# Kernel tuning notes

Measured on AMD Instinct MI355X. Metric: run time of the kernel, lower is better.

## Reference

```python
import jax, jax.numpy as jnp
import numpy as np

N_NODES = 100000
N_EDGES = 1600000
HIDDEN = 64


def setup_inputs() -> dict:
    key = jax.random.key(0)
    k1, k2, k3, k4 = jax.random.split(key, 4)
    x = jax.random.normal(k1, (N_NODES, HIDDEN), dtype=jnp.float32)
    A_rows = jax.random.randint(k2, (N_EDGES,), 0, N_NODES, dtype=jnp.int32)
    A_cols = jax.random.randint(k3, (N_EDGES,), 0, N_NODES, dtype=jnp.int32)
    A_vals = jax.random.uniform(k4, (N_EDGES,), dtype=jnp.float32)
    t = jnp.zeros((), dtype=jnp.float32)
    return {"t": t, "x": x, "A_rows": A_rows, "A_cols": A_cols, "A_vals": A_vals}


def reference(t, x, A_rows, A_cols, A_vals):
    # f = A @ x  (sparse COO SpMM): gather source features, scale, scatter-add to rows
    msgs = A_vals[:, None] * x[A_cols]           # [E, H]
    f = jax.ops.segment_sum(msgs, A_rows, num_segments=N_NODES)  # [N, H]
    # dropout rate is 0.0 -> identity; then ReLU
    return jax.nn.relu(f)
```

## Files before the change

### kernel.cpp

```cpp
#include <hip/hip_runtime.h>
#include <hip/hip_fp16.h>

#define N_NODES 100000
#define N_EDGES 1600000
#define HIDDEN 64
#define RPB 512
#define NCB ((N_NODES + RPB - 1) / RPB)
#define CAP 8960
#define R1_THREADS 512
#define R1_BATCH 6144
#define R1_PER_T (R1_BATCH / R1_THREADS)
#define FINE_SLOTS 9

__global__ void __launch_bounds__(256) conv_fp16_zero_kernel(const float4* __restrict__ x4,
                                                             ushort4* __restrict__ xh,
                                                             int* __restrict__ ccursor,
                                                             int n4) {
    if (blockIdx.x == 0 && threadIdx.x < NCB) ccursor[threadIdx.x] = 0;
    int i = blockIdx.x * blockDim.x + threadIdx.x;
    const int stride = gridDim.x * blockDim.x;
    for (; i < n4; i += stride) {
        const float4 v = x4[i];
        ushort4 q;
        q.x = __half_as_ushort(__float2half(v.x));
        q.y = __half_as_ushort(__float2half(v.y));
        q.z = __half_as_ushort(__float2half(v.z));
        q.w = __half_as_ushort(__float2half(v.w));
        xh[i] = q;
    }
}

__global__ void __launch_bounds__(R1_THREADS) coarse_scatter_pad_kernel(
        const int* __restrict__ rows, const int* __restrict__ cols,
        const float* __restrict__ vals, int* __restrict__ ccursor,
        int2* __restrict__ cbuf) {
    __shared__ int hist[NCB];
    __shared__ int base[NCB];
    const int t = threadIdx.x;
    const int b0 = blockIdx.x * R1_BATCH;
    for (int i = t; i < NCB; i += R1_THREADS) hist[i] = 0;
    __syncthreads();

    int  mb[R1_PER_T];
    int  rk[R1_PER_T];
    int2 md[R1_PER_T];
    #pragma unroll
    for (int k = 0; k < R1_PER_T; ++k) {
        const int e = b0 + k * R1_THREADS + t;
        mb[k] = -1;
        if (e < N_EDGES) {
            const int r = rows[e];
            mb[k] = r >> 9;
            md[k] = make_int2(((r & (RPB - 1)) << 17) | cols[e], __float_as_int(vals[e]));
            rk[k] = atomicAdd(&hist[mb[k]], 1);
        }
    }
    __syncthreads();
    for (int i = t; i < NCB; i += R1_THREADS) {
        const int c = hist[i];
        base[i] = c ? (i * CAP + atomicAdd(&ccursor[i], c)) : 0;
    }
    __syncthreads();
    #pragma unroll
    for (int k = 0; k < R1_PER_T; ++k)
        if (mb[k] >= 0) cbuf[base[mb[k]] + rk[k]] = md[k];
}

__global__ void __launch_bounds__(1024) fine_bucket2_kernel(
        const int2* __restrict__ cbuf, const int* __restrict__ ccursor,
        int* __restrict__ offs, int2* __restrict__ ebuf) {
    __shared__ int csc[2][256];
    __shared__ int s[2][RPB];
    __shared__ int lbase[RPB];
    const int b = blockIdx.x;
    const int t = threadIdx.x;

    if (t < 256) csc[0][t] = (t < NCB) ? ccursor[t] : 0;
    __syncthreads();
    int sc = 0;
    for (int off = 1; off < 256; off <<= 1) {
        if (t < 256) csc[1 - sc][t] = csc[sc][t] + (t >= off ? csc[sc][t - off] : 0);
        __syncthreads();
        sc ^= 1;
    }
    const int dst0 = b ? csc[sc][b - 1] : 0;
    const int cnt  = min(ccursor[b], CAP);
    const int src0 = b * CAP;
    if (b == 0 && t == 0) offs[N_NODES] = N_EDGES;

    if (t < RPB) s[0][t] = 0;
    __syncthreads();

    int  rw[FINE_SLOTS];
    int  rk[FINE_SLOTS];
    int2 md[FINE_SLOTS];
    #pragma unroll
    for (int k = 0; k < FINE_SLOTS; ++k) {
        const int i = k * 1024 + t;
        rw[k] = -1;
        if (i < cnt) {
            const int2 m = cbuf[src0 + i];
            const int row = (m.x >> 17) & (RPB - 1);
            rw[k] = row;
            md[k] = make_int2(m.x & 0x1FFFF, m.y);
            rk[k] = atomicAdd(&s[0][row], 1);
        }
    }
    __syncthreads();
    int src = 0;
    for (int off = 1; off < RPB; off <<= 1) {
        if (t < RPB) s[1 - src][t] = s[src][t] + (t >= off ? s[src][t - off] : 0);
        __syncthreads();
        src ^= 1;
    }
    if (t < RPB) {
        const int excl = dst0 + (t ? s[src][t - 1] : 0);
        lbase[t] = excl;
        const int row = (b << 9) + t;
        if (row < N_NODES) offs[row] = excl;
    }
    __syncthreads();
    #pragma unroll
    for (int k = 0; k < FINE_SLOTS; ++k)
        if (rw[k] >= 0) ebuf[lbase[rw[k]] + rk[k]] = md[k];
}

__global__ void __launch_bounds__(256) spmm_csr_relu_h4_kernel(
        const ushort4* __restrict__ xh, const int2* __restrict__ ebuf,
        const int* __restrict__ offs, float4* __restrict__ out4) {
    const int lane = threadIdx.x & 63;
    const int g = lane >> 4;
    const int h = lane & 15;
    const int wave = threadIdx.x >> 6;
    const int r = blockIdx.x * 4 + wave;
    if (r >= N_NODES) return;
    const int start = offs[r];
    const int n = offs[r + 1] - start;

    float4 acc = make_float4(0.f, 0.f, 0.f, 0.f);
    for (int base = 0; base < n; base += 64) {
        const int take = min(64, n - base);
        int2 m = make_int2(0, 0);
        if (base + lane < n) m = ebuf[start + base + lane];
        for (int j = 0; j < take; j += 16) {
            const int i0 = j + g, i1 = j + 4 + g, i2 = j + 8 + g, i3 = j + 12 + g;
            const int   c0 = __shfl(m.x, i0);
            const float v0 = __int_as_float(__shfl(m.y, i0));
            const int   c1 = __shfl(m.x, i1);
            const float v1 = __int_as_float(__shfl(m.y, i1));
            const int   c2 = __shfl(m.x, i2);
            const float v2 = __int_as_float(__shfl(m.y, i2));
            const int   c3 = __shfl(m.x, i3);
            const float v3 = __int_as_float(__shfl(m.y, i3));
            const ushort4 qa = xh[(size_t)c0 * 16 + h];
            const ushort4 qb = xh[(size_t)c1 * 16 + h];
            const ushort4 qc = xh[(size_t)c2 * 16 + h];
            const ushort4 qd = xh[(size_t)c3 * 16 + h];
            acc.x = fmaf(v0, __half2float(__ushort_as_half(qa.x)), acc.x);
            acc.y = fmaf(v0, __half2float(__ushort_as_half(qa.y)), acc.y);
            acc.z = fmaf(v0, __half2float(__ushort_as_half(qa.z)), acc.z);
            acc.w = fmaf(v0, __half2float(__ushort_as_half(qa.w)), acc.w);
            acc.x = fmaf(v1, __half2float(__ushort_as_half(qb.x)), acc.x);
            acc.y = fmaf(v1, __half2float(__ushort_as_half(qb.y)), acc.y);
            acc.z = fmaf(v1, __half2float(__ushort_as_half(qb.z)), acc.z);
            acc.w = fmaf(v1, __half2float(__ushort_as_half(qb.w)), acc.w);
            acc.x = fmaf(v2, __half2float(__ushort_as_half(qc.x)), acc.x);
            acc.y = fmaf(v2, __half2float(__ushort_as_half(qc.y)), acc.y);
            acc.z = fmaf(v2, __half2float(__ushort_as_half(qc.z)), acc.z);
            acc.w = fmaf(v2, __half2float(__ushort_as_half(qc.w)), acc.w);
            acc.x = fmaf(v3, __half2float(__ushort_as_half(qd.x)), acc.x);
            acc.y = fmaf(v3, __half2float(__ushort_as_half(qd.y)), acc.y);
            acc.z = fmaf(v3, __half2float(__ushort_as_half(qd.z)), acc.z);
            acc.w = fmaf(v3, __half2float(__ushort_as_half(qd.w)), acc.w);
        }
    }
    acc.x += __shfl_xor(acc.x, 16); acc.y += __shfl_xor(acc.y, 16);
    acc.z += __shfl_xor(acc.z, 16); acc.w += __shfl_xor(acc.w, 16);
    acc.x += __shfl_xor(acc.x, 32); acc.y += __shfl_xor(acc.y, 32);
    acc.z += __shfl_xor(acc.z, 32); acc.w += __shfl_xor(acc.w, 32);
    if (lane < 16) {
        float4 o;
        o.x = fmaxf(acc.x, 0.f); o.y = fmaxf(acc.y, 0.f);
        o.z = fmaxf(acc.z, 0.f); o.w = fmaxf(acc.w, 0.f);
        out4[(size_t)r * 16 + h] = o;
    }
}

__global__ void __launch_bounds__(256) spmm_csr_relu_f4_kernel(
        const float4* __restrict__ x4, const int2* __restrict__ ebuf,
        const int* __restrict__ offs, float4* __restrict__ out4) {
    const int lane = threadIdx.x & 63;
    const int g = lane >> 4;
    const int h = lane & 15;
    const int wave = threadIdx.x >> 6;
    const int r = blockIdx.x * 4 + wave;
    if (r >= N_NODES) return;
    const int start = offs[r];
    const int n = offs[r + 1] - start;

    float4 acc = make_float4(0.f, 0.f, 0.f, 0.f);
    for (int base = 0; base < n; base += 64) {
        const int take = min(64, n - base);
        int2 m = make_int2(0, 0);
        if (base + lane < n) m = ebuf[start + base + lane];
        for (int j = 0; j < take; j += 8) {
            const int j0 = j + g, j1 = j + 4 + g;
            const int   c0 = __shfl(m.x, j0);
            const float v0 = __int_as_float(__shfl(m.y, j0));
            const int   c1 = __shfl(m.x, j1);
            const float v1 = __int_as_float(__shfl(m.y, j1));
            const float4 a  = x4[(size_t)c0 * 16 + h];
            const float4 bq = x4[(size_t)c1 * 16 + h];
            acc.x = fmaf(v0, a.x, acc.x);  acc.y = fmaf(v0, a.y, acc.y);
            acc.z = fmaf(v0, a.z, acc.z);  acc.w = fmaf(v0, a.w, acc.w);
            acc.x = fmaf(v1, bq.x, acc.x); acc.y = fmaf(v1, bq.y, acc.y);
            acc.z = fmaf(v1, bq.z, acc.z); acc.w = fmaf(v1, bq.w, acc.w);
        }
    }
    acc.x += __shfl_xor(acc.x, 16); acc.y += __shfl_xor(acc.y, 16);
    acc.z += __shfl_xor(acc.z, 16); acc.w += __shfl_xor(acc.w, 16);
    acc.x += __shfl_xor(acc.x, 32); acc.y += __shfl_xor(acc.y, 32);
    acc.z += __shfl_xor(acc.z, 32); acc.w += __shfl_xor(acc.w, 32);
    if (lane < 16) {
        float4 o;
        o.x = fmaxf(acc.x, 0.f); o.y = fmaxf(acc.y, 0.f);
        o.z = fmaxf(acc.z, 0.f); o.w = fmaxf(acc.w, 0.f);
        out4[(size_t)r * 16 + h] = o;
    }
}

__global__ void spmm_scatter_kernel(const float* __restrict__ x,
                                    const int* __restrict__ rows,
                                    const int* __restrict__ cols,
                                    const float* __restrict__ vals,
                                    float* __restrict__ f) {
    const int lane = threadIdx.x & 63;
    const int wave = (blockIdx.x * blockDim.x + threadIdx.x) >> 6;
    const int nWaves = (gridDim.x * blockDim.x) >> 6;
    for (int e = wave; e < N_EDGES; e += nWaves)
        atomicAdd(&f[rows[e] * HIDDEN + lane], vals[e] * x[cols[e] * HIDDEN + lane]);
}
__global__ void relu_inplace_kernel(float4* __restrict__ f, int n4) {
    int i = blockIdx.x * blockDim.x + threadIdx.x;
    const int stride = gridDim.x * blockDim.x;
    for (; i < n4; i += stride) {
        float4 v = f[i];
        v.x = fmaxf(v.x, 0.0f); v.y = fmaxf(v.y, 0.0f);
        v.z = fmaxf(v.z, 0.0f); v.w = fmaxf(v.w, 0.0f);
        f[i] = v;
    }
}

extern "C" void kernel_launch(void* const* d_in, const int* in_sizes, int n_in,
                              void* d_out, int out_size, void* d_ws, size_t ws_size,
                              hipStream_t stream) {
    const float* x    = (const float*)d_in[1];
    const int*   rows = (const int*)d_in[2];
    const int*   cols = (const int*)d_in[3];
    const float* vals = (const float*)d_in[4];
    float* out = (float*)d_out;
    char* ws = (char*)d_ws;

    const size_t ccursor_off = 0;
    const size_t offs_off    = ccursor_off + (size_t)NCB * 4;
    size_t cbuf_off = offs_off + (size_t)(N_NODES + 1) * 4;
    cbuf_off = (cbuf_off + 15) & ~(size_t)15;
    const size_t ebuf_off = cbuf_off + (size_t)NCB * CAP * 8;
    const size_t xh_off   = ebuf_off + (size_t)N_EDGES * 8;
    const size_t ws_t1b = xh_off;
    const size_t ws_t1  = xh_off + (size_t)N_NODES * HIDDEN * 2;

    if (ws_size >= ws_t1b) {
        int*  ccursor = (int*)(ws + ccursor_off);
        int*  offs    = (int*)(ws + offs_off);
        int2* cbuf    = (int2*)(ws + cbuf_off);
        int2* ebuf    = (int2*)(ws + ebuf_off);
        const bool fp16_path = (ws_size >= ws_t1);

        if (fp16_path) {
            ushort4* xh = (ushort4*)(ws + xh_off);
            conv_fp16_zero_kernel<<<2048, 256, 0, stream>>>(
                (const float4*)x, xh, ccursor, N_NODES * HIDDEN / 4);
        } else {
            hipMemsetAsync(ccursor, 0, (size_t)NCB * 4, stream);
        }
        coarse_scatter_pad_kernel<<<(N_EDGES + R1_BATCH - 1) / R1_BATCH, R1_THREADS,
                                    0, stream>>>(rows, cols, vals, ccursor, cbuf);
        fine_bucket2_kernel<<<NCB, 1024, 0, stream>>>(cbuf, ccursor, offs, ebuf);
        if (fp16_path) {
            const ushort4* xh = (const ushort4*)(ws + xh_off);
            spmm_csr_relu_h4_kernel<<<N_NODES / 4, 256, 0, stream>>>(
                xh, ebuf, offs, (float4*)out);
        } else {
            spmm_csr_relu_f4_kernel<<<N_NODES / 4, 256, 0, stream>>>(
                (const float4*)x, ebuf, offs, (float4*)out);
        }
        return;
    }

    hipMemsetAsync(d_out, 0, (size_t)N_NODES * HIDDEN * sizeof(float), stream);
    spmm_scatter_kernel<<<2048, 256, 0, stream>>>(x, rows, cols, vals, out);
    relu_inplace_kernel<<<2048, 256, 0, stream>>>((float4*)d_out,
                                                  (N_NODES * HIDDEN) / 4);
}
```

Measured before the change: 94.58 us.

## Split fp16 features into column slices and process one slice per block

```diff
diff --git a/kernel.cpp b/kernel.cpp
--- a/kernel.cpp
+++ b/kernel.cpp
@@ -11,22 +11,25 @@
 #define R1_BATCH 6144
 #define R1_PER_T (R1_BATCH / R1_THREADS)
 #define FINE_SLOTS 9
-
-__global__ void __launch_bounds__(256) conv_fp16_zero_kernel(const float4* __restrict__ x4,
-                                                             ushort4* __restrict__ xh,
-                                                             int* __restrict__ ccursor,
-                                                             int n4) {
+#define NSLICE 4
+
+__global__ void __launch_bounds__(256) conv_sliced_zero_kernel(
+        const float4* __restrict__ x4, ushort4* __restrict__ xhs,
+        int* __restrict__ ccursor) {
     if (blockIdx.x == 0 && threadIdx.x < NCB) ccursor[threadIdx.x] = 0;
     int i = blockIdx.x * blockDim.x + threadIdx.x;
     const int stride = gridDim.x * blockDim.x;
+    const int n4 = N_NODES * 16;
     for (; i < n4; i += stride) {
         const float4 v = x4[i];
-        ushort4 q;
-        q.x = __half_as_ushort(__float2half(v.x));
-        q.y = __half_as_ushort(__float2half(v.y));
-        q.z = __half_as_ushort(__float2half(v.z));
-        q.w = __half_as_ushort(__float2half(v.w));
-        xh[i] = q;
+        const int node = i >> 4, q = i & 15;
+        const int s = q >> 2, w = q & 3;
+        ushort4 qq;
+        qq.x = __half_as_ushort(__float2half(v.x));
+        qq.y = __half_as_ushort(__float2half(v.y));
+        qq.z = __half_as_ushort(__float2half(v.z));
+        qq.w = __half_as_ushort(__float2half(v.w));
+        xhs[(size_t)s * (N_NODES * 4) + node * 4 + w] = qq;
     }
 }
 
@@ -125,64 +128,49 @@
         if (rw[k] >= 0) ebuf[lbase[rw[k]] + rk[k]] = md[k];
 }
 
-__global__ void __launch_bounds__(256) spmm_csr_relu_h4_kernel(
-        const ushort4* __restrict__ xh, const int2* __restrict__ ebuf,
-        const int* __restrict__ offs, float4* __restrict__ out4) {
+__global__ void __launch_bounds__(256) spmm_sliced_kernel(
+        const ushort2* __restrict__ xh, const int2* __restrict__ ebuf,
+        const int* __restrict__ offs, float2* __restrict__ out2) {
+    const int bid = blockIdx.x;
+    const int s = bid & 3;
+    const int rb = bid >> 2;
     const int lane = threadIdx.x & 63;
-    const int g = lane >> 4;
-    const int h = lane & 15;
     const int wave = threadIdx.x >> 6;
-    const int r = blockIdx.x * 4 + wave;
+    const int r = rb * 4 + wave;
     if (r >= N_NODES) return;
+    const int g = lane >> 3;
+    const int h = lane & 7;
     const int start = offs[r];
     const int n = offs[r + 1] - start;
-
-    float4 acc = make_float4(0.f, 0.f, 0.f, 0.f);
+    const ushort2* xs = xh + (size_t)s * (N_NODES * 8);
+
+    float ax = 0.f, ay = 0.f;
     for (int base = 0; base < n; base += 64) {
         const int take = min(64, n - base);
         int2 m = make_int2(0, 0);
         if (base + lane < n) m = ebuf[start + base + lane];
         for (int j = 0; j < take; j += 16) {
-            const int i0 = j + g, i1 = j + 4 + g, i2 = j + 8 + g, i3 = j + 12 + g;
+            const int i0 = j + g, i1 = j + 8 + g;
             const int   c0 = __shfl(m.x, i0);
             const float v0 = __int_as_float(__shfl(m.y, i0));
             const int   c1 = __shfl(m.x, i1);
             const float v1 = __int_as_float(__shfl(m.y, i1));
-            const int   c2 = __shfl(m.x, i2);
-            const float v2 = __int_as_float(__shfl(m.y, i2));
-            const int   c3 = __shfl(m.x, i3);
-            const float v3 = __int_as_float(__shfl(m.y, i3));
-            const ushort4 qa = xh[(size_t)c0 * 16 + h];
-            const ushort4 qb = xh[(size_t)c1 * 16 + h];
-            const ushort4 qc = xh[(size_t)c2 * 16 + h];
-            const ushort4 qd = xh[(size_t)c3 * 16 + h];
-            acc.x = fmaf(v0, __half2float(__ushort_as_half(qa.x)), acc.x);
-            acc.y = fmaf(v0, __half2float(__ushort_as_half(qa.y)), acc.y);
-            acc.z = fmaf(v0, __half2float(__ushort_as_half(qa.z)), acc.z);
-            acc.w = fmaf(v0, __half2float(__ushort_as_half(qa.w)), acc.w);
-            acc.x = fmaf(v1, __half2float(__ushort_as_half(qb.x)), acc.x);
-            acc.y = fmaf(v1, __half2float(__ushort_as_half(qb.y)), acc.y);
-            acc.z = fmaf(v1, __half2float(__ushort_as_half(qb.z)), acc.z);
-            acc.w = fmaf(v1, __half2float(__ushort_as_half(qb.w)), acc.w);
-            acc.x = fmaf(v2, __half2float(__ushort_as_half(qc.x)), acc.x);
-            acc.y = fmaf(v2, __half2float(__ushort_as_half(qc.y)), acc.y);
-            acc.z = fmaf(v2, __half2float(__ushort_as_half(qc.z)), acc.z);
-            acc.w = fmaf(v2, __half2float(__ushort_as_half(qc.w)), acc.w);
-            acc.x = fmaf(v3, __half2float(__ushort_as_half(qd.x)), acc.x);
-            acc.y = fmaf(v3, __half2float(__ushort_as_half(qd.y)), acc.y);
-            acc.z = fmaf(v3, __half2float(__ushort_as_half(qd.z)), acc.z);
-            acc.w = fmaf(v3, __half2float(__ushort_as_half(qd.w)), acc.w);
-        }
-    }
-    acc.x += __shfl_xor(acc.x, 16); acc.y += __shfl_xor(acc.y, 16);
-    acc.z += __shfl_xor(acc.z, 16); acc.w += __shfl_xor(acc.w, 16);
-    acc.x += __shfl_xor(acc.x, 32); acc.y += __shfl_xor(acc.y, 32);
-    acc.z += __shfl_xor(acc.z, 32); acc.w += __shfl_xor(acc.w, 32);
-    if (lane < 16) {
-        float4 o;
-        o.x = fmaxf(acc.x, 0.f); o.y = fmaxf(acc.y, 0.f);
-        o.z = fmaxf(acc.z, 0.f); o.w = fmaxf(acc.w, 0.f);
-        out4[(size_t)r * 16 + h] = o;
+            const ushort2 qa = xs[(size_t)(c0 & 0x1FFFF) * 8 + h];
+            const ushort2 qb = xs[(size_t)(c1 & 0x1FFFF) * 8 + h];
+            ax = fmaf(v0, __half2float(__ushort_as_half(qa.x)), ax);
+            ay = fmaf(v0, __half2float(__ushort_as_half(qa.y)), ay);
+            ax = fmaf(v1, __half2float(__ushort_as_half(qb.x)), ax);
+            ay = fmaf(v1, __half2float(__ushort_as_half(qb.y)), ay);
+        }
+    }
+    ax += __shfl_xor(ax, 8);  ay += __shfl_xor(ay, 8);
+    ax += __shfl_xor(ax, 16); ay += __shfl_xor(ay, 16);
+    ax += __shfl_xor(ax, 32); ay += __shfl_xor(ay, 32);
+    if (lane < 8) {
+        float2 o;
+        o.x = fmaxf(ax, 0.f);
+        o.y = fmaxf(ay, 0.f);
+        out2[(size_t)r * 32 + s * 8 + h] = o;
     }
 }
 
@@ -278,9 +266,9 @@
         const bool fp16_path = (ws_size >= ws_t1);
 
         if (fp16_path) {
-            ushort4* xh = (ushort4*)(ws + xh_off);
-            conv_fp16_zero_kernel<<<2048, 256, 0, stream>>>(
-                (const float4*)x, xh, ccursor, N_NODES * HIDDEN / 4);
+            ushort4* xhs = (ushort4*)(ws + xh_off);
+            conv_sliced_zero_kernel<<<2048, 256, 0, stream>>>(
+                (const float4*)x, xhs, ccursor);
         } else {
             hipMemsetAsync(ccursor, 0, (size_t)NCB * 4, stream);
         }
@@ -288,9 +276,9 @@
                                     0, stream>>>(rows, cols, vals, ccursor, cbuf);
         fine_bucket2_kernel<<<NCB, 1024, 0, stream>>>(cbuf, ccursor, offs, ebuf);
         if (fp16_path) {
-            const ushort4* xh = (const ushort4*)(ws + xh_off);
-            spmm_csr_relu_h4_kernel<<<N_NODES / 4, 256, 0, stream>>>(
-                xh, ebuf, offs, (float4*)out);
+            const ushort2* xh = (const ushort2*)(ws + xh_off);
+            spmm_sliced_kernel<<<(N_NODES / 4) * NSLICE, 256, 0, stream>>>(
+                xh, ebuf, offs, (float2*)out);
         } else {
             spmm_csr_relu_f4_kernel<<<N_NODES / 4, 256, 0, stream>>>(
                 (const float4*)x, ebuf, offs, (float4*)out);
```

Result: slower. 140.8 us (+48.8%).
